# Kernel optimization log

Hardware: AMD Instinct MI355X
Metric: run time of the kernel (lower is better)

The kernel has to match this reference:

```python
import jax, jax.numpy as jnp
import numpy as np

B, N, D, NUM_K = 128, 1024, 64, 8


def setup_inputs() -> dict:
    key = jax.random.key(0)
    k1, k2, k3 = jax.random.split(key, 3)
    nodes = jax.random.normal(k1, (B, N, D), dtype=jnp.float32)
    # xavier_uniform over (in_dims, in_dims) fan: bound = sqrt(6 / (N + N))
    bound = float(np.sqrt(6.0 / (N + N)))
    weight = jax.random.uniform(k2, (NUM_K, N, N), dtype=jnp.float32,
                                minval=-bound, maxval=bound)
    graph_shift = jax.random.normal(k3, (N, N), dtype=jnp.float32) / np.sqrt(N)
    return {"nodes": nodes, "weight": weight, "graph_shift": graph_shift}


def reference(nodes, weight, graph_shift):
    """Polynomial graph filter: out[b] = sum_k W_k @ S^k @ X_b.

    Since sum_k W_k S^k X = (sum_k W_k S^k) X, we fuse all taps into one
    N x N operator A, then apply a single batched GEMM over the batch.
    """
    n = nodes.shape[1]
    eye = jnp.eye(n, dtype=nodes.dtype)

    def step(S, Wk):
        # emit W_k @ S^k, carry S^{k+1}
        return S @ graph_shift, Wk @ S

    _, Mk = jax.lax.scan(step, eye, weight)   # [num_k, N, N]
    A = Mk.sum(axis=0)                        # fused filter operator [N, N]
    return jnp.einsum('nm,bmd->bnd', A, nodes)  # [B, N, D]
```

## Files before the change

### kernel.cpp

```cpp
#include <hip/hip_runtime.h>
#include <stdint.h>


#define NN 1024
#define NBATCH 128
#define DDIM 64

typedef float floatx4 __attribute__((ext_vector_type(4)));
typedef _Float16 f16x8 __attribute__((ext_vector_type(8)));
typedef unsigned short u16;

__device__ __forceinline__ u16 f2h(float f) {
  union { _Float16 h; u16 u; } v; v.h = (_Float16)f; return v.u;
}
__device__ __forceinline__ float h2f(u16 u) {
  union { _Float16 h; u16 u; } v; v.u = u; return (float)v.h;
}

__device__ __forceinline__ void gll16(const void* g, void* l) {
  __builtin_amdgcn_global_load_lds(
      (const __attribute__((address_space(1))) void*)g,
      (__attribute__((address_space(3))) void*)l, 16, 0, 0);
}

template <int N>
__device__ __forceinline__ void vm_wait() {
  static_assert(N == 0 || N == 4 || N == 6 || N == 8, "literal table");
  if constexpr (N == 0) asm volatile("s_waitcnt vmcnt(0)" ::: "memory");
  else if constexpr (N == 4) asm volatile("s_waitcnt vmcnt(4)" ::: "memory");
  else if constexpr (N == 6) asm volatile("s_waitcnt vmcnt(6)" ::: "memory");
  else if constexpr (N == 8) asm volatile("s_waitcnt vmcnt(8)" ::: "memory");
}
__device__ __forceinline__ void barrier() {
  asm volatile("s_barrier" ::: "memory");
}
__device__ __forceinline__ void lgkm0() {
  asm volatile("s_waitcnt lgkmcnt(0)" ::: "memory");
}

template <int ROWS>
__device__ __forceinline__ void stage64(const u16* __restrict__ g, u16* lds,
                                        int wave, int lane) {
  const int r = lane >> 3, c = lane & 7;
  const int sw = (c ^ r) * 8;
#pragma unroll
  for (int i = 0; i < ROWS / 32; ++i) {
    const int rb = wave * (ROWS / 4) + i * 8;
    gll16(g + (size_t)(rb + r) * NN + sw, lds + rb * 64);
  }
}

struct CvtJob { const float* src; u16* rm; u16* cm; };
struct CvtJobs { CvtJob j[5]; };

__global__ __launch_bounds__(256) void prep_kernel(CvtJobs jobs,
                                                   const float* __restrict__ X,
                                                   u16* __restrict__ XT) {
  __shared__ u16 T[64][72];
  const int bid = blockIdx.x;
  const int t = threadIdx.x;
  if (bid < 256) {
    const CvtJob jb = jobs.j[0];
    const int tr = bid >> 4, tc = bid & 15;
#pragma unroll
    for (int it = 0; it < 4; ++it) {
      int lr = (t >> 4) + it * 16;
      int lc4 = (t & 15) * 4;
      size_t gidx = (size_t)(tr * 64 + lr) * NN + tc * 64 + lc4;
      float4 f = *(const float4*)&jb.src[gidx];
      u16 h[4] = { f2h(f.x), f2h(f.y), f2h(f.z), f2h(f.w) };
      uint2 p;
      p.x = (uint32_t)h[0] | ((uint32_t)h[1] << 16);
      p.y = (uint32_t)h[2] | ((uint32_t)h[3] << 16);
      *(uint2*)&jb.rm[gidx] = p;
      T[lc4 + 0][lr] = h[0];
      T[lc4 + 1][lr] = h[1];
      T[lc4 + 2][lr] = h[2];
      T[lc4 + 3][lr] = h[3];
    }
    __syncthreads();
#pragma unroll
    for (int it = 0; it < 2; ++it) {
      int lc = (t >> 3) + it * 32;
      int lr8 = (t & 7) * 8;
      *(uint4*)&jb.cm[(size_t)(tc * 64 + lc) * NN + tr * 64 + lr8] =
          *(uint4*)&T[lc][lr8];
    }
  } else if (bid < 4352) {
    const int wb = bid - 256;
    const CvtJob jb = jobs.j[1 + (wb >> 10)];
    int idx4 = (wb & 1023) * 256 + t;
    int e = idx4 * 4;
    float4 f = ((const float4*)jb.src)[idx4];
    uint2 p;
    p.x = (uint32_t)f2h(f.x) | ((uint32_t)f2h(f.y) << 16);
    p.y = (uint32_t)f2h(f.z) | ((uint32_t)f2h(f.w) << 16);
    *(uint2*)&jb.rm[e] = p;
  } else {
    const int tb = bid - 4352;
    const int k0 = (tb & 15) * 64;
    const int b = tb >> 4;
#pragma unroll
    for (int it = 0; it < 4; ++it) {
      int kr = (t >> 4) + it * 16;
      int d4 = (t & 15) * 4;
      float4 f = *(const float4*)&X[((size_t)b * NN + k0 + kr) * DDIM + d4];
      T[d4 + 0][kr] = f2h(f.x);
      T[d4 + 1][kr] = f2h(f.y);
      T[d4 + 2][kr] = f2h(f.z);
      T[d4 + 3][kr] = f2h(f.w);
    }
    __syncthreads();
#pragma unroll
    for (int it = 0; it < 2; ++it) {
      int d = (t >> 3) + it * 32;
      int kc = (t & 7) * 8;
      *(uint4*)&XT[((size_t)b * DDIM + d) * NN + k0 + kc] = *(uint4*)&T[d][kc];
    }
  }
}

struct GemmJob {
  const u16* A;
  const u16* B;
  const float* addF;
  const u16* addH;
  u16* outRm;
  u16* outCm;
};
struct GemmJobs { GemmJob j[5]; };

template <int BM, int BN, int WM, int WN>
__global__ __launch_bounds__(256) void gemm_f16(GemmJobs jobs) {
  const GemmJob jb = jobs.j[blockIdx.z];
  __shared__ alignas(16) u16 As[3][BM * 64];
  __shared__ alignas(16) u16 Bs[3][BN * 64];
  const int t = threadIdx.x, wave = t >> 6, lane = t & 63;
  const int wm = wave / WN, wn = wave % WN;
  const int lm = lane & 15, q = lane >> 4;
  const int bm = blockIdx.x * BM, bn = blockIdx.y * BN;
  constexpr int MI = BM / (WM * 16), NI = BN / (WN * 16);
  constexpr int VMC = (BM + BN) / 32;
  floatx4 acc[MI][NI] = {};

  const u16* Ag = jb.A + (size_t)bm * NN;
  const u16* Bg = jb.B + (size_t)bn * NN;

  if (jb.addF) {
#pragma unroll
    for (int mi = 0; mi < MI; ++mi)
#pragma unroll
      for (int ni = 0; ni < NI; ++ni)
#pragma unroll
        for (int r = 0; r < 4; ++r) {
          int row = bm + wm * (BM / WM) + mi * 16 + q * 4 + r;
          int col = bn + wn * (BN / WN) + ni * 16 + lm;
          acc[mi][ni][r] = jb.addF[(size_t)row * NN + col];
        }
  } else if (jb.addH) {
#pragma unroll
    for (int mi = 0; mi < MI; ++mi)
#pragma unroll
      for (int ni = 0; ni < NI; ++ni)
#pragma unroll
        for (int r = 0; r < 4; ++r) {
          int row = bm + wm * (BM / WM) + mi * 16 + q * 4 + r;
          int col = bn + wn * (BN / WN) + ni * 16 + lm;
          acc[mi][ni][r] = h2f(jb.addH[(size_t)row * NN + col]);
        }
  }

  stage64<BM>(Ag, As[0], wave, lane);
  stage64<BN>(Bg, Bs[0], wave, lane);
  stage64<BM>(Ag + 64, As[1], wave, lane);
  stage64<BN>(Bg + 64, Bs[1], wave, lane);

  for (int kk = 0; kk < 16; ++kk) {
    const int cur = kk % 3;
    if (kk < 15) vm_wait<VMC>(); else vm_wait<0>();
    barrier();
    f16x8 af[2][MI], bf[2][NI];
#pragma unroll
    for (int ks = 0; ks < 2; ++ks) {
      const int st = ((ks * 4 + q) ^ (lm & 7)) * 8;
#pragma unroll
      for (int ni = 0; ni < NI; ++ni)
        bf[ks][ni] = *(const f16x8*)&Bs[cur][(wn * (BN / WN) + ni * 16 + lm) * 64 + st];
#pragma unroll
      for (int mi = 0; mi < MI; ++mi)
        af[ks][mi] = *(const f16x8*)&As[cur][(wm * (BM / WM) + mi * 16 + lm) * 64 + st];
    }
    if (kk + 2 < 16) {
      stage64<BM>(Ag + (kk + 2) * 64, As[(kk + 2) % 3], wave, lane);
      stage64<BN>(Bg + (kk + 2) * 64, Bs[(kk + 2) % 3], wave, lane);
    }
#pragma unroll
    for (int ks = 0; ks < 2; ++ks)
#pragma unroll
      for (int mi = 0; mi < MI; ++mi)
#pragma unroll
        for (int ni = 0; ni < NI; ++ni)
          acc[mi][ni] = __builtin_amdgcn_mfma_f32_16x16x32_f16(
              af[ks][mi], bf[ks][ni], acc[mi][ni], 0, 0, 0);
  }

#pragma unroll
  for (int mi = 0; mi < MI; ++mi)
#pragma unroll
    for (int ni = 0; ni < NI; ++ni) {
      int row0 = bm + wm * (BM / WM) + mi * 16 + q * 4;
      int col = bn + wn * (BN / WN) + ni * 16 + lm;
      u16 h[4];
#pragma unroll
      for (int r = 0; r < 4; ++r) h[r] = f2h(acc[mi][ni][r]);
      if (jb.outRm) {
#pragma unroll
        for (int r = 0; r < 4; ++r)
          jb.outRm[(size_t)(row0 + r) * NN + col] = h[r];
      }
      if (jb.outCm) {
        uint2 p;
        p.x = (uint32_t)h[0] | ((uint32_t)h[1] << 16);
        p.y = (uint32_t)h[2] | ((uint32_t)h[3] << 16);
        *(uint2*)&jb.outCm[(size_t)col * NN + row0] = p;
      }
    }
}

__global__ __launch_bounds__(256) void apply_gemm(const u16* __restrict__ A,
                                                  const u16* __restrict__ XT,
                                                  float* __restrict__ out) {
  __shared__ alignas(16) u16 As[2][128 * 64], Xs[2][128 * 64];
  const int t = threadIdx.x, wave = t >> 6, lane = t & 63;
  const int wm = wave >> 1, wn = wave & 1;
  const int lm = lane & 15, q = lane >> 4;
  const int bn = blockIdx.x * 128;
  const int bm = blockIdx.y * 128;
  floatx4 acc[4][4] = {};
  const u16* Ag = A + (size_t)bm * NN;
  const u16* Xg = XT + (size_t)bn * NN;

  stage64<128>(Ag, As[0], wave, lane);
  stage64<128>(Xg, Xs[0], wave, lane);

  for (int kt = 0; kt < 16; ++kt) {
    const int cur = kt & 1;
    if (kt + 1 < 16) {
      stage64<128>(Ag + (kt + 1) * 64, As[cur ^ 1], wave, lane);
      stage64<128>(Xg + (kt + 1) * 64, Xs[cur ^ 1], wave, lane);
      vm_wait<8>();
    } else {
      vm_wait<0>();
    }
    barrier();
#pragma unroll
    for (int ks = 0; ks < 2; ++ks) {
      const int st = ((ks * 4 + q) ^ (lm & 7)) * 8;
      f16x8 xf[4];
#pragma unroll
      for (int ni = 0; ni < 4; ++ni)
        xf[ni] = *(const f16x8*)&Xs[cur][(wn * 64 + ni * 16 + lm) * 64 + st];
#pragma unroll
      for (int mi = 0; mi < 4; ++mi) {
        f16x8 a = *(const f16x8*)&As[cur][(wm * 64 + mi * 16 + lm) * 64 + st];
#pragma unroll
        for (int ni = 0; ni < 4; ++ni)
          acc[mi][ni] = __builtin_amdgcn_mfma_f32_16x16x32_f16(a, xf[ni], acc[mi][ni], 0, 0, 0);
      }
    }
    lgkm0();
    barrier();
  }

#pragma unroll
  for (int mi = 0; mi < 4; ++mi)
#pragma unroll
    for (int ni = 0; ni < 4; ++ni)
#pragma unroll
      for (int r = 0; r < 4; ++r) {
        int row = bm + wm * 64 + mi * 16 + q * 4 + r;
        int col = bn + wn * 64 + ni * 16 + lm;
        out[((size_t)(col >> 6) * NN + row) * DDIM + (col & 63)] =
            acc[mi][ni][r];
      }
}

extern "C" void kernel_launch(void* const* d_in, const int* in_sizes, int n_in,
                              void* d_out, int out_size, void* d_ws, size_t ws_size,
                              hipStream_t stream) {
  const float* nodes  = (const float*)d_in[0];
  const float* weight = (const float*)d_in[1];
  const float* gs     = (const float*)d_in[2];
  float* out = (float*)d_out;
  u16* ws = (u16*)d_ws;
  const size_t MB = (size_t)NN * NN;
  auto buf = [&](int i) -> u16* { return ws + (size_t)i * MB; };

  u16* XT = buf(16);
  CvtJobs cv{};
  cv.j[0] = { gs,              buf(0), buf(1) };
  cv.j[1] = { weight + 1 * MB, buf(2), nullptr };
  cv.j[2] = { weight + 3 * MB, buf(3), nullptr };
  cv.j[3] = { weight + 5 * MB, buf(4), nullptr };
  cv.j[4] = { weight + 7 * MB, buf(5), nullptr };
  prep_kernel<<<dim3(6400), 256, 0, stream>>>(cv, nodes, XT);

  GemmJobs g1{};
  g1.j[0] = { buf(0), buf(1), nullptr,         nullptr, buf(6),  buf(7)  };
  g1.j[1] = { buf(2), buf(1), weight + 0 * MB, nullptr, buf(8),  nullptr };
  g1.j[2] = { buf(3), buf(1), weight + 2 * MB, nullptr, buf(9),  nullptr };
  g1.j[3] = { buf(4), buf(1), weight + 4 * MB, nullptr, buf(10), nullptr };
  g1.j[4] = { buf(5), buf(1), weight + 6 * MB, nullptr, buf(11), nullptr };
  gemm_f16<64, 128, 2, 2><<<dim3(16, 8, 5), 256, 0, stream>>>(g1);

  GemmJobs g2{};
  g2.j[0] = { buf(6),  buf(7), nullptr, nullptr, nullptr, buf(12) };
  g2.j[1] = { buf(9),  buf(7), nullptr, buf(8),  buf(13), nullptr };
  g2.j[2] = { buf(11), buf(7), nullptr, buf(10), buf(14), nullptr };
  gemm_f16<64, 64, 2, 2><<<dim3(16, 16, 3), 256, 0, stream>>>(g2);

  GemmJobs g3{};
  g3.j[0] = { buf(14), buf(12), nullptr, buf(13), buf(15), nullptr };
  gemm_f16<64, 64, 2, 2><<<dim3(16, 16, 1), 256, 0, stream>>>(g3);

  apply_gemm<<<dim3(64, 8), 256, 0, stream>>>(buf(15), XT, out);
}
```

Before: 173.2 us.

## Add dedicated level-1 GEMM kernel with direct A loads and fold X transpose in

Replaces the first-level batched GEMM with a new 128-thread kernel that uses 128x64 tiles, loads A fragments straight from global memory into registers with double buffering, and stages only B through LDS with a 3-deep pipeline. The X fp16 transpose work moves out of the prep kernel into extra blocks (z=5) of this new kernel, so it runs alongside the GEMM blocks. The aim is to shorten the prep kernel and raise overlap and per-wave MFMA density. The trade-off is uncoalesced-looking global A reads and fewer threads per block, and the transpose blocks loop serially over 16 tiles.

```diff
diff --git a/kernel.cpp b/kernel.cpp
--- a/kernel.cpp
+++ b/kernel.cpp
@@ -25,11 +25,12 @@
 
 template <int N>
 __device__ __forceinline__ void vm_wait() {
-  static_assert(N == 0 || N == 4 || N == 6 || N == 8, "literal table");
+  static_assert(N == 0 || N == 4 || N == 6 || N == 8 || N == 12, "literal table");
   if constexpr (N == 0) asm volatile("s_waitcnt vmcnt(0)" ::: "memory");
   else if constexpr (N == 4) asm volatile("s_waitcnt vmcnt(4)" ::: "memory");
   else if constexpr (N == 6) asm volatile("s_waitcnt vmcnt(6)" ::: "memory");
   else if constexpr (N == 8) asm volatile("s_waitcnt vmcnt(8)" ::: "memory");
+  else if constexpr (N == 12) asm volatile("s_waitcnt vmcnt(12)" ::: "memory");
 }
 __device__ __forceinline__ void barrier() {
   asm volatile("s_barrier" ::: "memory");
@@ -53,9 +54,7 @@
 struct CvtJob { const float* src; u16* rm; u16* cm; };
 struct CvtJobs { CvtJob j[5]; };
 
-__global__ __launch_bounds__(256) void prep_kernel(CvtJobs jobs,
-                                                   const float* __restrict__ X,
-                                                   u16* __restrict__ XT) {
+__global__ __launch_bounds__(256) void prep_kernel(CvtJobs jobs) {
   __shared__ u16 T[64][72];
   const int bid = blockIdx.x;
   const int t = threadIdx.x;
@@ -86,7 +85,7 @@
       *(uint4*)&jb.cm[(size_t)(tc * 64 + lc) * NN + tr * 64 + lr8] =
           *(uint4*)&T[lc][lr8];
     }
-  } else if (bid < 4352) {
+  } else {
     const int wb = bid - 256;
     const CvtJob jb = jobs.j[1 + (wb >> 10)];
     int idx4 = (wb & 1023) * 256 + t;
@@ -96,27 +95,6 @@
     p.x = (uint32_t)f2h(f.x) | ((uint32_t)f2h(f.y) << 16);
     p.y = (uint32_t)f2h(f.z) | ((uint32_t)f2h(f.w) << 16);
     *(uint2*)&jb.rm[e] = p;
-  } else {
-    const int tb = bid - 4352;
-    const int k0 = (tb & 15) * 64;
-    const int b = tb >> 4;
-#pragma unroll
-    for (int it = 0; it < 4; ++it) {
-      int kr = (t >> 4) + it * 16;
-      int d4 = (t & 15) * 4;
-      float4 f = *(const float4*)&X[((size_t)b * NN + k0 + kr) * DDIM + d4];
-      T[d4 + 0][kr] = f2h(f.x);
-      T[d4 + 1][kr] = f2h(f.y);
-      T[d4 + 2][kr] = f2h(f.z);
-      T[d4 + 3][kr] = f2h(f.w);
-    }
-    __syncthreads();
-#pragma unroll
-    for (int it = 0; it < 2; ++it) {
-      int d = (t >> 3) + it * 32;
-      int kc = (t & 7) * 8;
-      *(uint4*)&XT[((size_t)b * DDIM + d) * NN + k0 + kc] = *(uint4*)&T[d][kc];
-    }
   }
 }
 
@@ -129,6 +107,146 @@
   u16* outCm;
 };
 struct GemmJobs { GemmJob j[5]; };
+
+__global__ __launch_bounds__(128) void l1_kernel(GemmJobs jobs,
+                                                 const float* __restrict__ X,
+                                                 u16* __restrict__ XT) {
+  __shared__ alignas(16) u16 Bs[3][64 * 64];
+  __shared__ u16 T[64][72];
+  const int t = threadIdx.x;
+
+  if (blockIdx.z == 5) {
+    const int flat = blockIdx.x * 16 + blockIdx.y;
+    for (int i = 0; i < 16; ++i) {
+      const int tb = flat * 16 + i;
+      const int k0 = (tb & 15) * 64;
+      const int b = tb >> 4;
+#pragma unroll
+      for (int it = 0; it < 8; ++it) {
+        int kr = (t >> 4) + it * 8;
+        int d4 = (t & 15) * 4;
+        float4 f = *(const float4*)&X[((size_t)b * NN + k0 + kr) * DDIM + d4];
+        T[d4 + 0][kr] = f2h(f.x);
+        T[d4 + 1][kr] = f2h(f.y);
+        T[d4 + 2][kr] = f2h(f.z);
+        T[d4 + 3][kr] = f2h(f.w);
+      }
+      __syncthreads();
+#pragma unroll
+      for (int it = 0; it < 4; ++it) {
+        int d = (t >> 3) + it * 16;
+        int kc = (t & 7) * 8;
+        *(uint4*)&XT[((size_t)b * DDIM + d) * NN + k0 + kc] = *(uint4*)&T[d][kc];
+      }
+      __syncthreads();
+    }
+    return;
+  }
+
+  const GemmJob jb = jobs.j[blockIdx.z];
+  const int wave = t >> 6, lane = t & 63;
+  const int lm = lane & 15, q = lane >> 4;
+  const int r8 = lane >> 3, c8 = lane & 7;
+  const int sw = (c8 ^ r8) * 8;
+  const int bm = blockIdx.x * 128, bn = blockIdx.y * 64;
+  floatx4 acc[4][4] = {};
+
+  const u16* Bg = jb.B + (size_t)bn * NN;
+  const u16* Arow = jb.A + ((size_t)bm + wave * 64 + lm) * NN;
+
+  if (jb.addF) {
+#pragma unroll
+    for (int mi = 0; mi < 4; ++mi)
+#pragma unroll
+      for (int ni = 0; ni < 4; ++ni)
+#pragma unroll
+        for (int r = 0; r < 4; ++r) {
+          int row = bm + wave * 64 + mi * 16 + q * 4 + r;
+          int col = bn + ni * 16 + lm;
+          acc[mi][ni][r] = jb.addF[(size_t)row * NN + col];
+        }
+  } else if (jb.addH) {
+#pragma unroll
+    for (int mi = 0; mi < 4; ++mi)
+#pragma unroll
+      for (int ni = 0; ni < 4; ++ni)
+#pragma unroll
+        for (int r = 0; r < 4; ++r) {
+          int row = bm + wave * 64 + mi * 16 + q * 4 + r;
+          int col = bn + ni * 16 + lm;
+          acc[mi][ni][r] = h2f(jb.addH[(size_t)row * NN + col]);
+        }
+  }
+
+  auto stageB = [&](int kt, int buf) {
+#pragma unroll
+    for (int i = 0; i < 4; ++i) {
+      const int rb = wave * 32 + i * 8;
+      gll16(Bg + (size_t)(rb + r8) * NN + kt * 64 + sw, Bs[buf] + rb * 64);
+    }
+  };
+
+  f16x8 af[2][4][2];
+  auto loadA = [&](int kt, int buf) {
+#pragma unroll
+    for (int mi = 0; mi < 4; ++mi)
+#pragma unroll
+      for (int ks = 0; ks < 2; ++ks)
+        af[buf][mi][ks] = *(const f16x8*)(Arow + (size_t)mi * 16 * NN +
+                                          kt * 64 + ks * 32 + q * 8);
+  };
+
+  stageB(0, 0);
+  stageB(1, 1);
+  loadA(0, 0);
+
+#pragma unroll
+  for (int kk = 0; kk < 16; ++kk) {
+    const int cur = kk % 3;
+    vm_wait<12>();
+    barrier();
+    f16x8 bf[2][4];
+#pragma unroll
+    for (int ks = 0; ks < 2; ++ks) {
+      const int st = ((ks * 4 + q) ^ (lm & 7)) * 8;
+#pragma unroll
+      for (int ni = 0; ni < 4; ++ni)
+        bf[ks][ni] = *(const f16x8*)&Bs[cur][(ni * 16 + lm) * 64 + st];
+    }
+    if (kk + 2 < 16) stageB(kk + 2, (kk + 2) % 3);
+    if (kk + 1 < 16) loadA(kk + 1, (kk + 1) & 1);
+#pragma unroll
+    for (int ks = 0; ks < 2; ++ks)
+#pragma unroll
+      for (int mi = 0; mi < 4; ++mi)
+#pragma unroll
+        for (int ni = 0; ni < 4; ++ni)
+          acc[mi][ni] = __builtin_amdgcn_mfma_f32_16x16x32_f16(
+              af[kk & 1][mi][ks], bf[ks][ni], acc[mi][ni], 0, 0, 0);
+  }
+
+#pragma unroll
+  for (int mi = 0; mi < 4; ++mi)
+#pragma unroll
+    for (int ni = 0; ni < 4; ++ni) {
+      int row0 = bm + wave * 64 + mi * 16 + q * 4;
+      int col = bn + ni * 16 + lm;
+      u16 h[4];
+#pragma unroll
+      for (int r = 0; r < 4; ++r) h[r] = f2h(acc[mi][ni][r]);
+      if (jb.outRm) {
+#pragma unroll
+        for (int r = 0; r < 4; ++r)
+          jb.outRm[(size_t)(row0 + r) * NN + col] = h[r];
+      }
+      if (jb.outCm) {
+        uint2 p;
+        p.x = (uint32_t)h[0] | ((uint32_t)h[1] << 16);
+        p.y = (uint32_t)h[2] | ((uint32_t)h[3] << 16);
+        *(uint2*)&jb.outCm[(size_t)col * NN + row0] = p;
+      }
+    }
+}
 
 template <int BM, int BN, int WM, int WN>
 __global__ __launch_bounds__(256) void gemm_f16(GemmJobs jobs) {
@@ -303,7 +421,7 @@
   cv.j[2] = { weight + 3 * MB, buf(3), nullptr };
   cv.j[3] = { weight + 5 * MB, buf(4), nullptr };
   cv.j[4] = { weight + 7 * MB, buf(5), nullptr };
-  prep_kernel<<<dim3(6400), 256, 0, stream>>>(cv, nodes, XT);
+  prep_kernel<<<dim3(4352), 256, 0, stream>>>(cv);
 
   GemmJobs g1{};
   g1.j[0] = { buf(0), buf(1), nullptr,         nullptr, buf(6),  buf(7)  };
@@ -311,7 +429,7 @@
   g1.j[2] = { buf(3), buf(1), weight + 2 * MB, nullptr, buf(9),  nullptr };
   g1.j[3] = { buf(4), buf(1), weight + 4 * MB, nullptr, buf(10), nullptr };
   g1.j[4] = { buf(5), buf(1), weight + 6 * MB, nullptr, buf(11), nullptr };
-  gemm_f16<64, 128, 2, 2><<<dim3(16, 8, 5), 256, 0, stream>>>(g1);
+  l1_kernel<<<dim3(8, 16, 6), 128, 0, stream>>>(g1, nodes, XT);
 
   GemmJobs g2{};
   g2.j[0] = { buf(6),  buf(7), nullptr, nullptr, nullptr, buf(12) };
```

Result: slower. 176.7 us (+2.0%).

## Fuse fp32-to-fp16 weight conversion into first-stage GEMM A-operand loads

Applied to the files above, without the earlier changes.

Drops the separate pass that converted four weight matrices and the row-major graph shift to fp16. A new GEMM kernel loads A directly from fp32 global memory into registers, converts it in-register and double-buffers it across k-steps, while B is still staged through LDS. This removes a full write and re-read of fp16 copies, at the cost of twice the A-operand global traffic per GEMM tile and uncoalesced per-lane fp32 loads.

```diff
diff --git a/kernel.cpp b/kernel.cpp
--- a/kernel.cpp
+++ b/kernel.cpp
@@ -25,11 +25,11 @@
 
 template <int N>
 __device__ __forceinline__ void vm_wait() {
-  static_assert(N == 0 || N == 4 || N == 6 || N == 8, "literal table");
+  static_assert(N == 0 || N == 4 || N == 8 || N == 12, "literal table");
   if constexpr (N == 0) asm volatile("s_waitcnt vmcnt(0)" ::: "memory");
   else if constexpr (N == 4) asm volatile("s_waitcnt vmcnt(4)" ::: "memory");
-  else if constexpr (N == 6) asm volatile("s_waitcnt vmcnt(6)" ::: "memory");
   else if constexpr (N == 8) asm volatile("s_waitcnt vmcnt(8)" ::: "memory");
+  else if constexpr (N == 12) asm volatile("s_waitcnt vmcnt(12)" ::: "memory");
 }
 __device__ __forceinline__ void barrier() {
   asm volatile("s_barrier" ::: "memory");
@@ -50,54 +50,35 @@
   }
 }
 
-struct CvtJob { const float* src; u16* rm; u16* cm; };
-struct CvtJobs { CvtJob j[5]; };
-
-__global__ __launch_bounds__(256) void prep_kernel(CvtJobs jobs,
+__global__ __launch_bounds__(256) void prep_kernel(const float* __restrict__ gs,
+                                                   u16* __restrict__ Scm,
                                                    const float* __restrict__ X,
                                                    u16* __restrict__ XT) {
   __shared__ u16 T[64][72];
   const int bid = blockIdx.x;
   const int t = threadIdx.x;
   if (bid < 256) {
-    const CvtJob jb = jobs.j[0];
     const int tr = bid >> 4, tc = bid & 15;
 #pragma unroll
     for (int it = 0; it < 4; ++it) {
       int lr = (t >> 4) + it * 16;
       int lc4 = (t & 15) * 4;
-      size_t gidx = (size_t)(tr * 64 + lr) * NN + tc * 64 + lc4;
-      float4 f = *(const float4*)&jb.src[gidx];
-      u16 h[4] = { f2h(f.x), f2h(f.y), f2h(f.z), f2h(f.w) };
-      uint2 p;
-      p.x = (uint32_t)h[0] | ((uint32_t)h[1] << 16);
-      p.y = (uint32_t)h[2] | ((uint32_t)h[3] << 16);
-      *(uint2*)&jb.rm[gidx] = p;
-      T[lc4 + 0][lr] = h[0];
-      T[lc4 + 1][lr] = h[1];
-      T[lc4 + 2][lr] = h[2];
-      T[lc4 + 3][lr] = h[3];
+      float4 f = *(const float4*)&gs[(size_t)(tr * 64 + lr) * NN + tc * 64 + lc4];
+      T[lc4 + 0][lr] = f2h(f.x);
+      T[lc4 + 1][lr] = f2h(f.y);
+      T[lc4 + 2][lr] = f2h(f.z);
+      T[lc4 + 3][lr] = f2h(f.w);
     }
     __syncthreads();
 #pragma unroll
     for (int it = 0; it < 2; ++it) {
       int lc = (t >> 3) + it * 32;
       int lr8 = (t & 7) * 8;
-      *(uint4*)&jb.cm[(size_t)(tc * 64 + lc) * NN + tr * 64 + lr8] =
+      *(uint4*)&Scm[(size_t)(tc * 64 + lc) * NN + tr * 64 + lr8] =
           *(uint4*)&T[lc][lr8];
     }
-  } else if (bid < 4352) {
-    const int wb = bid - 256;
-    const CvtJob jb = jobs.j[1 + (wb >> 10)];
-    int idx4 = (wb & 1023) * 256 + t;
-    int e = idx4 * 4;
-    float4 f = ((const float4*)jb.src)[idx4];
-    uint2 p;
-    p.x = (uint32_t)f2h(f.x) | ((uint32_t)f2h(f.y) << 16);
-    p.y = (uint32_t)f2h(f.z) | ((uint32_t)f2h(f.w) << 16);
-    *(uint2*)&jb.rm[e] = p;
   } else {
-    const int tb = bid - 4352;
+    const int tb = bid - 256;
     const int k0 = (tb & 15) * 64;
     const int b = tb >> 4;
 #pragma unroll
@@ -118,6 +99,110 @@
       *(uint4*)&XT[((size_t)b * DDIM + d) * NN + k0 + kc] = *(uint4*)&T[d][kc];
     }
   }
+}
+
+struct A32Job {
+  const float* A32;
+  const u16* B;
+  const float* addF;
+  u16* outRm;
+  u16* outCm;
+};
+struct A32Jobs { A32Job j[5]; };
+
+__global__ __launch_bounds__(256, 3) void gemm_a32(A32Jobs jobs) {
+  const A32Job jb = jobs.j[blockIdx.z];
+  __shared__ alignas(16) u16 Bs[3][128 * 64];
+  const int t = threadIdx.x, wave = t >> 6, lane = t & 63;
+  const int wm = wave >> 1, wn = wave & 1;
+  const int lm = lane & 15, q = lane >> 4;
+  const int bm = blockIdx.x * 64, bn = blockIdx.y * 128;
+  floatx4 acc[2][4] = {};
+
+  const u16* Bg = jb.B + (size_t)bn * NN;
+  const float* Ar = jb.A32 + ((size_t)bm + wm * 32 + lm) * NN + q * 8;
+
+  if (jb.addF) {
+#pragma unroll
+    for (int mi = 0; mi < 2; ++mi)
+#pragma unroll
+      for (int ni = 0; ni < 4; ++ni)
+#pragma unroll
+        for (int r = 0; r < 4; ++r) {
+          int row = bm + wm * 32 + mi * 16 + q * 4 + r;
+          int col = bn + wn * 64 + ni * 16 + lm;
+          acc[mi][ni][r] = jb.addF[(size_t)row * NN + col];
+        }
+  }
+
+  f16x8 af[2][2][2];
+  auto loadA = [&](int kt, int par) {
+#pragma unroll
+    for (int mi = 0; mi < 2; ++mi)
+#pragma unroll
+      for (int ks = 0; ks < 2; ++ks) {
+        const float* p = Ar + (size_t)mi * 16 * NN + kt * 64 + ks * 32;
+        float4 x = *(const float4*)p;
+        float4 y = *(const float4*)(p + 4);
+        f16x8 f;
+        f[0] = (_Float16)x.x; f[1] = (_Float16)x.y;
+        f[2] = (_Float16)x.z; f[3] = (_Float16)x.w;
+        f[4] = (_Float16)y.x; f[5] = (_Float16)y.y;
+        f[6] = (_Float16)y.z; f[7] = (_Float16)y.w;
+        af[par][mi][ks] = f;
+      }
+  };
+
+  stage64<128>(Bg, Bs[0], wave, lane);
+  stage64<128>(Bg + 64, Bs[1], wave, lane);
+  loadA(0, 0);
+
+#pragma unroll
+  for (int kk = 0; kk < 16; ++kk) {
+    const int cur = kk % 3;
+    if (kk < 15) vm_wait<12>(); else vm_wait<0>();
+    barrier();
+    f16x8 bf[2][4];
+#pragma unroll
+    for (int ks = 0; ks < 2; ++ks) {
+      const int st = ((ks * 4 + q) ^ (lm & 7)) * 8;
+#pragma unroll
+      for (int ni = 0; ni < 4; ++ni)
+        bf[ks][ni] = *(const f16x8*)&Bs[cur][(wn * 64 + ni * 16 + lm) * 64 + st];
+    }
+    if (kk + 2 < 16) stage64<128>(Bg + (kk + 2) * 64, Bs[(kk + 2) % 3], wave, lane);
+    if (kk + 1 < 16) loadA(kk + 1, (kk + 1) & 1);
+#pragma unroll
+    for (int ks = 0; ks < 2; ++ks)
+#pragma unroll
+      for (int mi = 0; mi < 2; ++mi)
+#pragma unroll
+        for (int ni = 0; ni < 4; ++ni)
+          acc[mi][ni] = __builtin_amdgcn_mfma_f32_16x16x32_f16(
+              af[kk & 1][mi][ks], bf[ks][ni], acc[mi][ni], 0, 0, 0);
+  }
+
+#pragma unroll
+  for (int mi = 0; mi < 2; ++mi)
+#pragma unroll
+    for (int ni = 0; ni < 4; ++ni) {
+      int row0 = bm + wm * 32 + mi * 16 + q * 4;
+      int col = bn + wn * 64 + ni * 16 + lm;
+      u16 h[4];
+#pragma unroll
+      for (int r = 0; r < 4; ++r) h[r] = f2h(acc[mi][ni][r]);
+      if (jb.outRm) {
+#pragma unroll
+        for (int r = 0; r < 4; ++r)
+          jb.outRm[(size_t)(row0 + r) * NN + col] = h[r];
+      }
+      if (jb.outCm) {
+        uint2 p;
+        p.x = (uint32_t)h[0] | ((uint32_t)h[1] << 16);
+        p.y = (uint32_t)h[2] | ((uint32_t)h[3] << 16);
+        *(uint2*)&jb.outCm[(size_t)col * NN + row0] = p;
+      }
+    }
 }
 
 struct GemmJob {
@@ -297,21 +382,15 @@
   auto buf = [&](int i) -> u16* { return ws + (size_t)i * MB; };
 
   u16* XT = buf(16);
-  CvtJobs cv{};
-  cv.j[0] = { gs,              buf(0), buf(1) };
-  cv.j[1] = { weight + 1 * MB, buf(2), nullptr };
-  cv.j[2] = { weight + 3 * MB, buf(3), nullptr };
-  cv.j[3] = { weight + 5 * MB, buf(4), nullptr };
-  cv.j[4] = { weight + 7 * MB, buf(5), nullptr };
-  prep_kernel<<<dim3(6400), 256, 0, stream>>>(cv, nodes, XT);
-
-  GemmJobs g1{};
-  g1.j[0] = { buf(0), buf(1), nullptr,         nullptr, buf(6),  buf(7)  };
-  g1.j[1] = { buf(2), buf(1), weight + 0 * MB, nullptr, buf(8),  nullptr };
-  g1.j[2] = { buf(3), buf(1), weight + 2 * MB, nullptr, buf(9),  nullptr };
-  g1.j[3] = { buf(4), buf(1), weight + 4 * MB, nullptr, buf(10), nullptr };
-  g1.j[4] = { buf(5), buf(1), weight + 6 * MB, nullptr, buf(11), nullptr };
-  gemm_f16<64, 128, 2, 2><<<dim3(16, 8, 5), 256, 0, stream>>>(g1);
+  prep_kernel<<<dim3(256 + 2048), 256, 0, stream>>>(gs, buf(1), nodes, XT);
+
+  A32Jobs g1{};
+  g1.j[0] = { gs,              buf(1), nullptr,         buf(6),  buf(7)  };
+  g1.j[1] = { weight + 1 * MB, buf(1), weight + 0 * MB, buf(8),  nullptr };
+  g1.j[2] = { weight + 3 * MB, buf(1), weight + 2 * MB, buf(9),  nullptr };
+  g1.j[3] = { weight + 5 * MB, buf(1), weight + 4 * MB, buf(10), nullptr };
+  g1.j[4] = { weight + 7 * MB, buf(1), weight + 6 * MB, buf(11), nullptr };
+  gemm_a32<<<dim3(16, 8, 5), 256, 0, stream>>>(g1);
 
   GemmJobs g2{};
   g2.j[0] = { buf(6),  buf(7), nullptr, nullptr, nullptr, buf(12) };
```

Measured after the change: 201.0 us. 16.0% more time.
